# Optimization experiments

Measured on AMD Instinct MI355X. Metric: run time of the kernel, lower is better.

The kernel has to match this reference:

```python
import jax, jax.numpy as jnp
import numpy as np

H = 16
EPS = 1e-6
AUX_COEF = 0.01
TOPK = 2


def _rmsnorm(x, w):
    ms = jnp.mean(x * x, axis=-1, keepdims=True)
    return x * jax.lax.rsqrt(ms + EPS) * w


def _rope(t, cos, sin):
    # t: [B,H,T,hd]; cos/sin: [T, hd//2]
    half = t.shape[-1] // 2
    t1, t2 = t[..., :half], t[..., half:]
    return jnp.concatenate([t1 * cos - t2 * sin, t1 * sin + t2 * cos], axis=-1)


def setup_inputs() -> dict:
    key = jax.random.key(0)
    ks = jax.random.split(key, 16)
    B, T, D = 2, 1024, 1024
    E, I = 8, 4096
    s = lambda k, shp, fan: jax.random.normal(k, shp, dtype=jnp.float32) * (1.0 / np.sqrt(fan))
    return {
        "x": jax.random.normal(ks[0], (B, T, D), dtype=jnp.float32),
        "qkv_w": s(ks[1], (3 * D, D), D),
        "qkv_b": jnp.zeros((3 * D,), jnp.float32),
        "out_w": s(ks[2], (D, D), D),
        "out_b": jnp.zeros((D,), jnp.float32),
        "ln1_w": jnp.ones((D,), jnp.float32),
        "ln2_w": jnp.ones((D,), jnp.float32),
        "gate_w": s(ks[3], (E, D), D),
        "ew1": s(ks[4], (E, I, D), D),
        "eb1": jnp.zeros((E, I), jnp.float32),
        "ew2": s(ks[5], (E, D, I), I),
        "eb2": jnp.zeros((E, D), jnp.float32),
        "ew3": s(ks[6], (E, I, D), D),
        "eb3": jnp.zeros((E, I), jnp.float32),
    }


def _attention(x, qkv_w, qkv_b, out_w, out_b):
    B, T, D = x.shape
    hd = D // H
    half = hd // 2
    qkv = (x @ qkv_w.T + qkv_b).reshape(B, T, H, 3, hd)
    q = jnp.transpose(qkv[..., 0, :], (0, 2, 1, 3))  # [B,H,T,hd]
    k = jnp.transpose(qkv[..., 1, :], (0, 2, 1, 3))
    v = jnp.transpose(qkv[..., 2, :], (0, 2, 1, 3))
    theta = 1.0 / (10000.0 ** (jnp.arange(half, dtype=jnp.float32) / half))
    freq = jnp.arange(T, dtype=jnp.float32)[:, None] * theta[None, :]  # [T,half]
    cos, sin = jnp.cos(freq), jnp.sin(freq)
    q = _rope(q, cos, sin)
    k = _rope(k, cos, sin)
    # NOTE: original scales by embed_dim**-0.5 (not head_dim**-0.5)
    scale = D ** (-0.5)
    scores = jnp.einsum("bhqd,bhkd->bhqk", q, k) * scale
    mask = jnp.triu(jnp.full((T, T), -1e9, dtype=scores.dtype), k=1)
    w = jax.nn.softmax(scores + mask, axis=-1)
    attn = jnp.einsum("bhqk,bhkd->bhqd", w, v)
    attn = jnp.transpose(attn, (0, 2, 1, 3)).reshape(B, T, D)
    return attn @ out_w.T + out_b


def _moe(x, gate_w, ew1, eb1, ew2, eb2, ew3, eb3):
    B, T, D = x.shape
    E = gate_w.shape[0]
    xf = x.reshape(-1, D)  # [N,D]
    N = xf.shape[0]
    probs = jax.nn.softmax(xf @ gate_w.T, axis=-1)  # [N,E]
    topk_vals, topk_idx = jax.lax.top_k(probs, TOPK)
    oh = jax.nn.one_hot(topk_idx, E, dtype=xf.dtype)  # [N,K,E]
    gates = jnp.sum(oh * topk_vals[..., None], axis=1)  # [N,E] dense gate, zero off top-k
    # per-expert SwiGLU over all tokens, combined with sparse gates
    h = jax.nn.silu(jnp.einsum("nd,eid->nei", xf, ew1) + eb1) * (
        jnp.einsum("nd,eid->nei", xf, ew3) + eb3
    )  # [N,E,I]
    out_e = jnp.einsum("nei,edi->ned", h, ew2) + eb2  # [N,E,D]
    y = jnp.einsum("ned,ne->nd", out_e, gates)
    counts = jnp.sum(oh, axis=(0, 1))  # bincount of routed assignments
    f = counts / (N * TOPK)
    P = jnp.mean(probs, axis=0)
    aux = AUX_COEF * E * jnp.dot(f, P)
    return y.reshape(B, T, D), aux


def reference(x, qkv_w, qkv_b, out_w, out_b, ln1_w, ln2_w, gate_w, ew1, eb1, ew2, eb2, ew3, eb3):
    h1 = x + _attention(_rmsnorm(x, ln1_w), qkv_w, qkv_b, out_w, out_b)
    y, aux = _moe(_rmsnorm(h1, ln2_w), gate_w, ew1, eb1, ew2, eb2, ew3, eb3)
    return h1 + y, aux
```

## Files before the change

### kernel.cpp

```cpp
#include <hip/hip_runtime.h>
#include <cstdint>
#include <cstddef>
#include <math.h>

#define T_SEQ  1024
#define DMODEL 1024
#define NHEAD  16
#define HDIM   64
#define NEXP   8
#define IDIM   4096
#define NTOK   2048
#define NSLOT  4096

typedef short bf16x8 __attribute__((ext_vector_type(8)));
typedef short s16x4  __attribute__((ext_vector_type(4)));
typedef float floatx4 __attribute__((ext_vector_type(4)));
typedef unsigned int uintx4 __attribute__((ext_vector_type(4)));

__device__ __forceinline__ float bf2f(short s) {
  return __uint_as_float(((unsigned)(unsigned short)s) << 16);
}
__device__ __forceinline__ short f2bf(float f) {
  unsigned u = __float_as_uint(f);
  unsigned r = (u + 0x7FFFu + ((u >> 16) & 1u)) >> 16;
  return (short)r;
}
__device__ __forceinline__ unsigned cvt_pk_bf16(float lo, float hi) {
  unsigned r;
  asm("v_cvt_pk_bf16_f32 %0, %1, %2" : "=v"(r) : "v"(lo), "v"(hi));
  return r;
}
__device__ __forceinline__ uintx4 pack8_bf16(floatx4 a, floatx4 b) {
  uintx4 u;
  u[0] = cvt_pk_bf16(a[0], a[1]);
  u[1] = cvt_pk_bf16(a[2], a[3]);
  u[2] = cvt_pk_bf16(b[0], b[1]);
  u[3] = cvt_pk_bf16(b[2], b[3]);
  return u;
}
__device__ __forceinline__ void split8(const float* x, uintx4& hi, uintx4& lo) {
  #pragma unroll
  for (int i = 0; i < 4; i++) {
    unsigned h = cvt_pk_bf16(x[2*i], x[2*i+1]);
    hi[i] = h;
    float r0 = x[2*i]   - __uint_as_float(h << 16);
    float r1 = x[2*i+1] - __uint_as_float(h & 0xffff0000u);
    lo[i] = cvt_pk_bf16(r0, r1);
  }
}

__global__ __launch_bounds__(256) void rmsnorm_f32_kernel(
    const float* __restrict__ x, const float* __restrict__ w, float* __restrict__ out) {
  int row = blockIdx.x, tid = threadIdx.x;
  const floatx4* xr = (const floatx4*)(x + (size_t)row * DMODEL);
  floatx4 v = xr[tid];
  float ss = v[0]*v[0] + v[1]*v[1] + v[2]*v[2] + v[3]*v[3];
  #pragma unroll
  for (int off = 32; off > 0; off >>= 1) ss += __shfl_xor(ss, off);
  __shared__ float wsum[4];
  int wid = tid >> 6;
  if ((tid & 63) == 0) wsum[wid] = ss;
  __syncthreads();
  float tot = wsum[0] + wsum[1] + wsum[2] + wsum[3];
  float r = rsqrtf(tot * (1.0f / DMODEL) + 1e-6f);
  floatx4 wv = ((const floatx4*)w)[tid];
  floatx4 o;
  o[0] = v[0]*r*wv[0]; o[1] = v[1]*r*wv[1];
  o[2] = v[2]*r*wv[2]; o[3] = v[3]*r*wv[3];
  ((floatx4*)(out + (size_t)row * DMODEL))[tid] = o;
}

__global__ __launch_bounds__(256) void rmsnorm_bf16_kernel(
    const float* __restrict__ x, const float* __restrict__ w, short* __restrict__ out) {
  int row = blockIdx.x, tid = threadIdx.x;
  const floatx4* xr = (const floatx4*)(x + (size_t)row * DMODEL);
  floatx4 v = xr[tid];
  float ss = v[0]*v[0] + v[1]*v[1] + v[2]*v[2] + v[3]*v[3];
  #pragma unroll
  for (int off = 32; off > 0; off >>= 1) ss += __shfl_xor(ss, off);
  __shared__ float wsum[4];
  int wid = tid >> 6;
  if ((tid & 63) == 0) wsum[wid] = ss;
  __syncthreads();
  float tot = wsum[0] + wsum[1] + wsum[2] + wsum[3];
  float r = rsqrtf(tot * (1.0f / DMODEL) + 1e-6f);
  floatx4 wv = ((const floatx4*)w)[tid];
  s16x4 o;
  o[0] = f2bf(v[0]*r*wv[0]); o[1] = f2bf(v[1]*r*wv[1]);
  o[2] = f2bf(v[2]*r*wv[2]); o[3] = f2bf(v[3]*r*wv[3]);
  *(s16x4*)(out + (size_t)row * DMODEL + tid*4) = o;
}

template<int RESID>
__global__ __launch_bounds__(256) void gemm_3bf16(
    const float* __restrict__ A, const float* __restrict__ W,
    const float* __restrict__ bias, const float* __restrict__ resid,
    float* __restrict__ C, int N, int K) {
  __shared__ __attribute__((aligned(16))) short Ahi[2][64*40];
  __shared__ __attribute__((aligned(16))) short Alo[2][64*40];
  __shared__ __attribute__((aligned(16))) short Whi[2][64*40];
  __shared__ __attribute__((aligned(16))) short Wlo[2][64*40];
  int tid = threadIdx.x, lane = tid & 63, wid = tid >> 6;
  int wm = wid >> 1, wn = wid & 1;
  int m0 = blockIdx.y * 64, n0 = blockIdx.x * 64;
  floatx4 zero4 = {0.f,0.f,0.f,0.f};
  floatx4 acc[2][2];
  #pragma unroll
  for (int mi = 0; mi < 2; mi++)
    #pragma unroll
    for (int nj = 0; nj < 2; nj++) acc[mi][nj] = zero4;

  int ar = tid >> 2, ak = (tid & 3) * 8;
  const float* Ap = A + (size_t)(m0 + ar) * K + ak;
  const float* Wp = W + (size_t)(n0 + ar) * K + ak;
  int rsel = lane & 15, kseg = (lane >> 4) * 8;

  {
    float abuf[8], wbuf[8];
    *(floatx4*)(abuf)     = *(const floatx4*)(Ap);
    *(floatx4*)(abuf + 4) = *(const floatx4*)(Ap + 4);
    *(floatx4*)(wbuf)     = *(const floatx4*)(Wp);
    *(floatx4*)(wbuf + 4) = *(const floatx4*)(Wp + 4);
    uintx4 ahi, alo, whi, wlo;
    split8(abuf, ahi, alo);
    split8(wbuf, whi, wlo);
    *(uintx4*)(&Ahi[0][ar*40 + ak]) = ahi;
    *(uintx4*)(&Alo[0][ar*40 + ak]) = alo;
    *(uintx4*)(&Whi[0][ar*40 + ak]) = whi;
    *(uintx4*)(&Wlo[0][ar*40 + ak]) = wlo;
  }
  __syncthreads();

  for (int kk = 0; kk < K; kk += 32) {
    int cur = (kk >> 5) & 1;
    int nxt = cur ^ 1;
    bool more = (kk + 32 < K);
    float nab[8], nwb[8];
    if (more) {
      *(floatx4*)(nab)     = *(const floatx4*)(Ap + kk + 32);
      *(floatx4*)(nab + 4) = *(const floatx4*)(Ap + kk + 36);
      *(floatx4*)(nwb)     = *(const floatx4*)(Wp + kk + 32);
      *(floatx4*)(nwb + 4) = *(const floatx4*)(Wp + kk + 36);
    }
    bf16x8 afh[2], afl[2], wfh[2], wfl[2];
    #pragma unroll
    for (int mi = 0; mi < 2; mi++) {
      int row = (wm*32 + mi*16 + rsel)*40 + kseg;
      afh[mi] = *(const bf16x8*)(&Ahi[cur][row]);
      afl[mi] = *(const bf16x8*)(&Alo[cur][row]);
    }
    #pragma unroll
    for (int nj = 0; nj < 2; nj++) {
      int row = (wn*32 + nj*16 + rsel)*40 + kseg;
      wfh[nj] = *(const bf16x8*)(&Whi[cur][row]);
      wfl[nj] = *(const bf16x8*)(&Wlo[cur][row]);
    }
    #pragma unroll
    for (int mi = 0; mi < 2; mi++)
      #pragma unroll
      for (int nj = 0; nj < 2; nj++) {
        acc[mi][nj] = __builtin_amdgcn_mfma_f32_16x16x32_bf16(afl[mi], wfh[nj], acc[mi][nj], 0, 0, 0);
        acc[mi][nj] = __builtin_amdgcn_mfma_f32_16x16x32_bf16(afh[mi], wfl[nj], acc[mi][nj], 0, 0, 0);
        acc[mi][nj] = __builtin_amdgcn_mfma_f32_16x16x32_bf16(afh[mi], wfh[nj], acc[mi][nj], 0, 0, 0);
      }
    if (more) {
      uintx4 ahi, alo, whi, wlo;
      split8(nab, ahi, alo);
      split8(nwb, whi, wlo);
      *(uintx4*)(&Ahi[nxt][ar*40 + ak]) = ahi;
      *(uintx4*)(&Alo[nxt][ar*40 + ak]) = alo;
      *(uintx4*)(&Whi[nxt][ar*40 + ak]) = whi;
      *(uintx4*)(&Wlo[nxt][ar*40 + ak]) = wlo;
    }
    __syncthreads();
  }
  int rj = (lane >> 4) * 4, cn = lane & 15;
  #pragma unroll
  for (int mi = 0; mi < 2; mi++) {
    #pragma unroll
    for (int nj = 0; nj < 2; nj++) {
      int n = n0 + wn*32 + nj*16 + cn;
      float bn = bias[n];
      #pragma unroll
      for (int j = 0; j < 4; j++) {
        int m = m0 + wm*32 + mi*16 + rj + j;
        float v = acc[mi][nj][j] + bn;
        if (RESID) v += resid[(size_t)m * N + n];
        C[(size_t)m * N + n] = v;
      }
    }
  }
}

__global__ void rope_table_kernel(float* __restrict__ cost, float* __restrict__ sint) {
  int t = blockIdx.x, d = threadIdx.x;
  double theta = pow(10000.0, -(double)d / 32.0);
  double f = (double)t * theta;
  cost[t*32 + d] = (float)cos(f);
  sint[t*32 + d] = (float)sin(f);
}

__global__ __launch_bounds__(256) void rope_kernel(
    const float* __restrict__ qkv, const float* __restrict__ cost, const float* __restrict__ sint,
    float* __restrict__ qr, float* __restrict__ kr) {
  int wid = threadIdx.x >> 6, lane = threadIdx.x & 63;
  int idx = blockIdx.x * 4 + wid;
  int h = idx & 15, n = idx >> 4;
  int t = n & (T_SEQ - 1), b = n >> 10;
  const float* base = qkv + (size_t)n * 3072 + h * 192;
  int d2 = lane & 31;
  float c = cost[t*32 + d2], s = sint[t*32 + d2];
  float q1 = base[d2],      q2 = base[d2 + 32];
  float k1 = base[64 + d2], k2 = base[96 + d2];
  float qo = (lane < 32) ? (q1*c - q2*s) : (q1*s + q2*c);
  float ko = (lane < 32) ? (k1*c - k2*s) : (k1*s + k2*c);
  size_t orow = ((size_t)(b*NHEAD + h) * T_SEQ + t) * HDIM;
  qr[orow + lane] = qo;
  kr[orow + lane] = ko;
}

__global__ __launch_bounds__(256) void vtrans_kernel(
    const float* __restrict__ qkvf, float* __restrict__ vrT) {
  __shared__ __attribute__((aligned(16))) float tile[64][68];
  int bh = blockIdx.x, t0 = blockIdx.y * 64;
  int b = bh >> 4, h = bh & 15;
  int tid = threadIdx.x;
  int r = tid >> 2, seg = (tid & 3) * 16;
  const float* src = qkvf + ((size_t)(b*T_SEQ + t0 + r))*3072 + h*192 + 128 + seg;
  floatx4 v0 = *(const floatx4*)(src);
  floatx4 v1 = *(const floatx4*)(src + 4);
  floatx4 v2 = *(const floatx4*)(src + 8);
  floatx4 v3 = *(const floatx4*)(src + 12);
  *(floatx4*)(&tile[r][seg])      = v0;
  *(floatx4*)(&tile[r][seg + 4])  = v1;
  *(floatx4*)(&tile[r][seg + 8])  = v2;
  *(floatx4*)(&tile[r][seg + 12]) = v3;
  __syncthreads();
  int dr = r, tseg = seg;
  floatx4 o0, o1, o2, o3;
  #pragma unroll
  for (int i = 0; i < 4; i++) {
    o0[i] = tile[tseg + i][dr];
    o1[i] = tile[tseg + 4 + i][dr];
    o2[i] = tile[tseg + 8 + i][dr];
    o3[i] = tile[tseg + 12 + i][dr];
  }
  float* dst = vrT + ((size_t)(bh*HDIM + dr))*T_SEQ + t0 + tseg;
  *(floatx4*)(dst)      = o0;
  *(floatx4*)(dst + 4)  = o1;
  *(floatx4*)(dst + 8)  = o2;
  *(floatx4*)(dst + 12) = o3;
}

__global__ __launch_bounds__(256) void attn_mfma_kernel(
    const float* __restrict__ qr_, const float* __restrict__ kr_,
    const float* __restrict__ vrT_, float* __restrict__ attno) {
  __shared__ __attribute__((aligned(16))) short Qhi[64*72];
  __shared__ __attribute__((aligned(16))) short Qlo[64*72];
  __shared__ __attribute__((aligned(16))) short Khi[64*72];
  __shared__ __attribute__((aligned(16))) short Klo[64*72];
  __shared__ __attribute__((aligned(16))) short Vhi[64*72];
  __shared__ __attribute__((aligned(16))) short Vlo[64*72];
  __shared__ __attribute__((aligned(16))) unsigned Pp[64*68];
  int tid = threadIdx.x, lane = tid & 63, w = tid >> 6;
  int bh = blockIdx.x;
  int qt = 15 - (int)blockIdx.y;
  int q0 = qt * 64;
  int b = bh >> 4, h = bh & 15;
  const float* Qb  = qr_  + ((size_t)bh * T_SEQ + q0) * HDIM;
  const float* Kb  = kr_  + (size_t)bh * T_SEQ * HDIM;
  const float* Vtb = vrT_ + (size_t)bh * HDIM * T_SEQ;

  int srow = tid >> 2, sseg = (tid & 3) * 16;
  {
    const float* src = Qb + srow*HDIM + sseg;
    float b0[8], b1[8];
    *(floatx4*)(b0)   = *(const floatx4*)(src);
    *(floatx4*)(b0+4) = *(const floatx4*)(src + 4);
    *(floatx4*)(b1)   = *(const floatx4*)(src + 8);
    *(floatx4*)(b1+4) = *(const floatx4*)(src + 12);
    uintx4 h0, l0, h1, l1;
    split8(b0, h0, l0); split8(b1, h1, l1);
    *(uintx4*)(&Qhi[srow*72 + sseg])     = h0;
    *(uintx4*)(&Qhi[srow*72 + sseg + 8]) = h1;
    *(uintx4*)(&Qlo[srow*72 + sseg])     = l0;
    *(uintx4*)(&Qlo[srow*72 + sseg + 8]) = l1;
  }

  int rsel = lane & 15, kseg = (lane >> 4) * 8, cl = lane & 15;
  int rbase = w*16 + (lane >> 4) * 4;
  const float scale = 0.03125f;
  float mrow[4] = {-1e30f,-1e30f,-1e30f,-1e30f};
  float lrow[4] = {0.f,0.f,0.f,0.f};
  floatx4 zero4 = {0.f,0.f,0.f,0.f};
  floatx4 Of[4];
  #pragma unroll
  for (int f = 0; f < 4; f++) Of[f] = zero4;

  int ntiles = qt + 1;
  for (int kt = 0; kt < ntiles; kt++) {
    int kbase = kt << 6;
    const float* kp = Kb  + (size_t)(kbase + srow)*HDIM + sseg;
    const float* vp = Vtb + (size_t)srow*T_SEQ + kbase + sseg;
    float kb0[8], kb1[8], vb0[8], vb1[8];
    *(floatx4*)(kb0)   = *(const floatx4*)(kp);
    *(floatx4*)(kb0+4) = *(const floatx4*)(kp + 4);
    *(floatx4*)(kb1)   = *(const floatx4*)(kp + 8);
    *(floatx4*)(kb1+4) = *(const floatx4*)(kp + 12);
    *(floatx4*)(vb0)   = *(const floatx4*)(vp);
    *(floatx4*)(vb0+4) = *(const floatx4*)(vp + 4);
    *(floatx4*)(vb1)   = *(const floatx4*)(vp + 8);
    *(floatx4*)(vb1+4) = *(const floatx4*)(vp + 12);
    __syncthreads();
    {
      uintx4 h0, l0, h1, l1;
      split8(kb0, h0, l0); split8(kb1, h1, l1);
      *(uintx4*)(&Khi[srow*72 + sseg])     = h0;
      *(uintx4*)(&Khi[srow*72 + sseg + 8]) = h1;
      *(uintx4*)(&Klo[srow*72 + sseg])     = l0;
      *(uintx4*)(&Klo[srow*72 + sseg + 8]) = l1;
      split8(vb0, h0, l0); split8(vb1, h1, l1);
      *(uintx4*)(&Vhi[srow*72 + sseg])     = h0;
      *(uintx4*)(&Vhi[srow*72 + sseg + 8]) = h1;
      *(uintx4*)(&Vlo[srow*72 + sseg])     = l0;
      *(uintx4*)(&Vlo[srow*72 + sseg + 8]) = l1;
    }
    __syncthreads();
    floatx4 sf[4];
    #pragma unroll
    for (int f = 0; f < 4; f++) sf[f] = zero4;
    #pragma unroll
    for (int c = 0; c < 2; c++) {
      int ko = c*32 + kseg;
      bf16x8 qh = *(const bf16x8*)(&Qhi[(w*16 + rsel)*72 + ko]);
      bf16x8 ql = *(const bf16x8*)(&Qlo[(w*16 + rsel)*72 + ko]);
      #pragma unroll
      for (int f = 0; f < 4; f++) {
        bf16x8 kh = *(const bf16x8*)(&Khi[(f*16 + rsel)*72 + ko]);
        bf16x8 kl = *(const bf16x8*)(&Klo[(f*16 + rsel)*72 + ko]);
        sf[f] = __builtin_amdgcn_mfma_f32_16x16x32_bf16(ql, kh, sf[f], 0, 0, 0);
        sf[f] = __builtin_amdgcn_mfma_f32_16x16x32_bf16(qh, kl, sf[f], 0, 0, 0);
        sf[f] = __builtin_amdgcn_mfma_f32_16x16x32_bf16(qh, kh, sf[f], 0, 0, 0);
      }
    }
    float pm[4] = {-1e30f,-1e30f,-1e30f,-1e30f};
    #pragma unroll
    for (int f = 0; f < 4; f++) {
      int col = kbase + f*16 + cl;
      #pragma unroll
      for (int j = 0; j < 4; j++) {
        float s = sf[f][j];
        s = (col <= q0 + rbase + j) ? s*scale : -1e30f;
        sf[f][j] = s;
        pm[j] = fmaxf(pm[j], s);
      }
    }
    #pragma unroll
    for (int off = 1; off < 16; off <<= 1)
      #pragma unroll
      for (int j = 0; j < 4; j++) pm[j] = fmaxf(pm[j], __shfl_xor(pm[j], off));
    float sc[4], rs[4] = {0.f,0.f,0.f,0.f};
    #pragma unroll
    for (int j = 0; j < 4; j++) {
      float mn = fmaxf(mrow[j], pm[j]);
      sc[j] = __expf(mrow[j] - mn);
      mrow[j] = mn;
    }
    #pragma unroll
    for (int f = 0; f < 4; f++) {
      #pragma unroll
      for (int j = 0; j < 4; j++) {
        float p = (sf[f][j] > -1e29f) ? __expf(sf[f][j] - mrow[j]) : 0.f;
        rs[j] += p;
        unsigned hp = cvt_pk_bf16(p, 0.f);
        float ph = __uint_as_float(hp << 16);
        unsigned lp = cvt_pk_bf16(p - ph, 0.f);
        Pp[(rbase + j)*68 + f*16 + cl] = (hp << 16) | (lp & 0xffffu);
      }
    }
    #pragma unroll
    for (int off = 1; off < 16; off <<= 1)
      #pragma unroll
      for (int j = 0; j < 4; j++) rs[j] += __shfl_xor(rs[j], off);
    #pragma unroll
    for (int j = 0; j < 4; j++) lrow[j] = lrow[j]*sc[j] + rs[j];
    #pragma unroll
    for (int f = 0; f < 4; f++)
      #pragma unroll
      for (int j = 0; j < 4; j++) Of[f][j] *= sc[j];
    __syncthreads();
    #pragma unroll
    for (int c = 0; c < 2; c++) {
      int prow = (w*16 + rsel)*68 + c*32 + kseg;
      uintx4 d0 = *(const uintx4*)(&Pp[prow]);
      uintx4 d1 = *(const uintx4*)(&Pp[prow + 4]);
      uintx4 phw, plw;
      phw[0] = (d0[0] >> 16) | (d0[1] & 0xffff0000u);
      phw[1] = (d0[2] >> 16) | (d0[3] & 0xffff0000u);
      phw[2] = (d1[0] >> 16) | (d1[1] & 0xffff0000u);
      phw[3] = (d1[2] >> 16) | (d1[3] & 0xffff0000u);
      plw[0] = (d0[0] & 0xffffu) | (d0[1] << 16);
      plw[1] = (d0[2] & 0xffffu) | (d0[3] << 16);
      plw[2] = (d1[0] & 0xffffu) | (d1[1] << 16);
      plw[3] = (d1[2] & 0xffffu) | (d1[3] << 16);
      bf16x8 Ph = *(bf16x8*)&phw;
      bf16x8 Pl = *(bf16x8*)&plw;
      int ko = c*32 + kseg;
      #pragma unroll
      for (int f = 0; f < 4; f++) {
        bf16x8 vh = *(const bf16x8*)(&Vhi[(f*16 + rsel)*72 + ko]);
        bf16x8 vl = *(const bf16x8*)(&Vlo[(f*16 + rsel)*72 + ko]);
        Of[f] = __builtin_amdgcn_mfma_f32_16x16x32_bf16(Pl, vh, Of[f], 0, 0, 0);
        Of[f] = __builtin_amdgcn_mfma_f32_16x16x32_bf16(Ph, vl, Of[f], 0, 0, 0);
        Of[f] = __builtin_amdgcn_mfma_f32_16x16x32_bf16(Ph, vh, Of[f], 0, 0, 0);
      }
    }
  }
  #pragma unroll
  for (int j = 0; j < 4; j++) {
    float inv = 1.0f / lrow[j];
    size_t rowoff = ((size_t)(b*T_SEQ + q0 + rbase + j))*DMODEL + h*HDIM;
    #pragma unroll
    for (int f = 0; f < 4; f++)
      attno[rowoff + f*16 + cl] = Of[f][j] * inv;
  }
}

__global__ __launch_bounds__(64) void gate_kernel(
    const float* __restrict__ h1, const float* __restrict__ lnw, const float* __restrict__ gw,
    float* __restrict__ probs, int* __restrict__ pair, float* __restrict__ gpair,
    int* __restrict__ counts) {
  int n = blockIdx.x, lane = threadIdx.x;
  const float* xp = h1 + (size_t)n * DMODEL + lane*16;
  float xv[16];
  double ss = 0.0;
  #pragma unroll
  for (int j = 0; j < 16; j++) { xv[j] = xp[j]; ss += (double)xv[j] * (double)xv[j]; }
  #pragma unroll
  for (int off = 32; off > 0; off >>= 1) ss += __shfl_xor(ss, off);
  double r = 1.0 / sqrt(ss * (1.0 / DMODEL) + 1e-6);
  const float* wp = lnw + lane*16;
  double xf[16];
  #pragma unroll
  for (int j = 0; j < 16; j++) xf[j] = (double)xv[j] * r * (double)wp[j];
  double logit[8];
  #pragma unroll
  for (int e = 0; e < 8; e++) {
    const float* g = gw + e*DMODEL + lane*16;
    double acc = 0.0;
    #pragma unroll
    for (int j = 0; j < 16; j++) acc += xf[j] * (double)g[j];
    logit[e] = acc;
  }
  #pragma unroll
  for (int e = 0; e < 8; e++)
    #pragma unroll
    for (int off = 32; off > 0; off >>= 1) logit[e] += __shfl_xor(logit[e], off);
  double mxl = logit[0];
  #pragma unroll
  for (int e = 1; e < 8; e++) mxl = fmax(mxl, logit[e]);
  double p[8], Z = 0.0;
  #pragma unroll
  for (int e = 0; e < 8; e++) { p[e] = exp(logit[e] - mxl); Z += p[e]; }
  double invZ = 1.0 / Z;
  #pragma unroll
  for (int e = 0; e < 8; e++) p[e] *= invZ;
  int e0 = 0; double b0 = p[0];
  #pragma unroll
  for (int e = 1; e < 8; e++) if (p[e] > b0) { b0 = p[e]; e0 = e; }
  int e1 = -1; double b1 = -1.0;
  #pragma unroll
  for (int e = 0; e < 8; e++) if (e != e0 && p[e] > b1) { b1 = p[e]; e1 = e; }
  if (lane == 0) {
    #pragma unroll
    for (int e = 0; e < 8; e++) probs[n*8 + e] = (float)p[e];
    pair[2*n] = e0; pair[2*n+1] = e1;
    gpair[2*n] = (float)b0; gpair[2*n+1] = (float)b1;
    atomicAdd(&counts[e0], 1);
    atomicAdd(&counts[e1], 1);
  }
}

__global__ void offsets_kernel(const int* __restrict__ counts, int* __restrict__ off,
                               int* __restrict__ cursor) {
  if (threadIdx.x == 0) {
    int a = 0;
    for (int e = 0; e < 8; e++) { off[e] = a; cursor[e] = a; a += counts[e]; }
    off[8] = a;
  }
}

__global__ __launch_bounds__(256) void scatter_kernel(
    const int* __restrict__ pair, const float* __restrict__ gpair, int* __restrict__ cursor,
    int* __restrict__ tok_of_slot, float* __restrict__ gate_of_slot, int* __restrict__ slot_of_tok) {
  int n = blockIdx.x * 256 + threadIdx.x;
  int e0 = pair[2*n], e1 = pair[2*n+1];
  int s0 = atomicAdd(&cursor[e0], 1);
  tok_of_slot[s0] = n; gate_of_slot[s0] = gpair[2*n];   slot_of_tok[2*n] = s0;
  int s1 = atomicAdd(&cursor[e1], 1);
  tok_of_slot[s1] = n; gate_of_slot[s1] = gpair[2*n+1]; slot_of_tok[2*n+1] = s1;
}

__global__ __launch_bounds__(256) void aux_kernel(
    const float* __restrict__ probs, const int* __restrict__ counts, float* __restrict__ outaux) {
  __shared__ double sm[256];
  int t = threadIdx.x;
  int e = t & 7, base = t >> 3;
  double acc = 0.0;
  for (int n = base; n < NTOK; n += 32) acc += (double)probs[n*8 + e];
  sm[t] = acc;
  __syncthreads();
  if (t < 8) {
    double s = 0.0;
    for (int g = 0; g < 32; g++) s += sm[g*8 + t];
    sm[t] = s;
  }
  __syncthreads();
  if (t == 0) {
    double aux = 0.0;
    for (int ee = 0; ee < 8; ee++)
      aux += ((double)counts[ee] * (1.0 / (NTOK*2))) * (sm[ee] * (1.0 / NTOK));
    outaux[0] = (float)(0.08 * aux);
  }
}

__global__ __launch_bounds__(256) void moe13_kernel(
    const short* __restrict__ xn2,
    const float* __restrict__ ew1, const float* __restrict__ eb1,
    const float* __restrict__ ew3, const float* __restrict__ eb3,
    const int* __restrict__ counts, const int* __restrict__ off,
    const int* __restrict__ tok_of_slot, short* __restrict__ hbuf) {
  int e = blockIdx.z;
  int Me = counts[e];
  int m0 = blockIdx.y * 128;
  if (m0 >= Me) return;
  int base = off[e];
  int i0 = blockIdx.x * 64;
  __shared__ __attribute__((aligned(16))) short As[2][128*40];
  __shared__ __attribute__((aligned(16))) short W1s[2][64*40];
  __shared__ __attribute__((aligned(16))) short W3s[2][64*40];
  int tid = threadIdx.x, lane = tid & 63, wid = tid >> 6;
  int wm = wid >> 1, wn = wid & 1;
  floatx4 zero4 = {0.f,0.f,0.f,0.f};
  floatx4 acc1[4][2], acc3[4][2];
  #pragma unroll
  for (int mi = 0; mi < 4; mi++)
    #pragma unroll
    for (int nj = 0; nj < 2; nj++) { acc1[mi][nj] = zero4; acc3[mi][nj] = zero4; }

  int ar = tid >> 1, ak = (tid & 1) * 8;
  int am = m0 + ar;
  bool aval = (am < Me);
  const short* Ag = xn2 + (size_t)(aval ? tok_of_slot[base + am] : 0) * DMODEL;
  int wr = tid >> 2, wk = (tid & 3) * 8;
  const float* W1g = ew1 + ((size_t)e*IDIM + i0 + wr)*DMODEL + wk;
  const float* W3g = ew3 + ((size_t)e*IDIM + i0 + wr)*DMODEL + wk;
  int rsel = lane & 15, kseg = (lane >> 4) * 8;

  {
    bf16x8 a0 = {0,0,0,0,0,0,0,0}, a1 = {0,0,0,0,0,0,0,0};
    if (aval) {
      a0 = *(const bf16x8*)(Ag + ak);
      a1 = *(const bf16x8*)(Ag + ak + 16);
    }
    floatx4 u0 = *(const floatx4*)(W1g);
    floatx4 u1 = *(const floatx4*)(W1g + 4);
    floatx4 v0 = *(const floatx4*)(W3g);
    floatx4 v1 = *(const floatx4*)(W3g + 4);
    *(bf16x8*)(&As[0][ar*40 + ak])      = a0;
    *(bf16x8*)(&As[0][ar*40 + ak + 16]) = a1;
    *(uintx4*)(&W1s[0][wr*40 + wk]) = pack8_bf16(u0, u1);
    *(uintx4*)(&W3s[0][wr*40 + wk]) = pack8_bf16(v0, v1);
  }
  __syncthreads();

  for (int kk = 0; kk < DMODEL; kk += 32) {
    int cur = (kk >> 5) & 1;
    int nxt = cur ^ 1;
    bool more = (kk + 32 < DMODEL);
    bf16x8 na0 = {0,0,0,0,0,0,0,0}, na1 = {0,0,0,0,0,0,0,0};
    floatx4 nu0, nu1, nv0, nv1;
    if (more) {
      if (aval) {
        na0 = *(const bf16x8*)(Ag + kk + 32 + ak);
        na1 = *(const bf16x8*)(Ag + kk + 32 + ak + 16);
      }
      nu0 = *(const floatx4*)(W1g + kk + 32);
      nu1 = *(const floatx4*)(W1g + kk + 36);
      nv0 = *(const floatx4*)(W3g + kk + 32);
      nv1 = *(const floatx4*)(W3g + kk + 36);
    }
    bf16x8 af[4], w1f[2], w3f[2];
    #pragma unroll
    for (int mi = 0; mi < 4; mi++)
      af[mi] = *(const bf16x8*)(&As[cur][(wm*64 + mi*16 + rsel)*40 + kseg]);
    #pragma unroll
    for (int nj = 0; nj < 2; nj++) {
      w1f[nj] = *(const bf16x8*)(&W1s[cur][(wn*32 + nj*16 + rsel)*40 + kseg]);
      w3f[nj] = *(const bf16x8*)(&W3s[cur][(wn*32 + nj*16 + rsel)*40 + kseg]);
    }
    #pragma unroll
    for (int mi = 0; mi < 4; mi++)
      #pragma unroll
      for (int nj = 0; nj < 2; nj++) {
        acc1[mi][nj] = __builtin_amdgcn_mfma_f32_16x16x32_bf16(af[mi], w1f[nj], acc1[mi][nj], 0, 0, 0);
        acc3[mi][nj] = __builtin_amdgcn_mfma_f32_16x16x32_bf16(af[mi], w3f[nj], acc3[mi][nj], 0, 0, 0);
      }
    if (more) {
      *(bf16x8*)(&As[nxt][ar*40 + ak])      = na0;
      *(bf16x8*)(&As[nxt][ar*40 + ak + 16]) = na1;
      *(uintx4*)(&W1s[nxt][wr*40 + wk]) = pack8_bf16(nu0, nu1);
      *(uintx4*)(&W3s[nxt][wr*40 + wk]) = pack8_bf16(nv0, nv1);
    }
    __syncthreads();
  }
  int rj = (lane >> 4) * 4, cn = lane & 15;
  #pragma unroll
  for (int mi = 0; mi < 4; mi++) {
    #pragma unroll
    for (int nj = 0; nj < 2; nj++) {
      int i = i0 + wn*32 + nj*16 + cn;
      float be1 = eb1[e*IDIM + i], be3 = eb3[e*IDIM + i];
      #pragma unroll
      for (int j = 0; j < 4; j++) {
        int m = m0 + wm*64 + mi*16 + rj + j;
        if (m < Me) {
          float a = acc1[mi][nj][j] + be1;
          float b = acc3[mi][nj][j] + be3;
          float hval = (a / (1.f + __expf(-a))) * b;
          hbuf[(size_t)(base + m)*IDIM + i] = f2bf(hval);
        }
      }
    }
  }
}

__global__ __launch_bounds__(256) void moe2_kernel(
    const short* __restrict__ hbuf, const float* __restrict__ ew2, const float* __restrict__ eb2,
    const int* __restrict__ counts, const int* __restrict__ off,
    const float* __restrict__ gate_of_slot,
    float* __restrict__ y0, float* __restrict__ y1) {
  int e = blockIdx.z;
  int Me = counts[e];
  int m0 = blockIdx.y * 128;
  if (m0 >= Me) return;
  int base = off[e];
  int n0 = (blockIdx.x & 7) * 128;
  int khalf = blockIdx.x >> 3;
  int kbeg = khalf * (IDIM/2);
  __shared__ __attribute__((aligned(16))) short As[2][128*40];
  __shared__ __attribute__((aligned(16))) short Ws[2][128*40];
  int tid = threadIdx.x, lane = tid & 63, wid = tid >> 6;
  int wm = wid >> 1, wn = wid & 1;
  floatx4 zero4 = {0.f,0.f,0.f,0.f};
  floatx4 acc[4][4];
  #pragma unroll
  for (int mi = 0; mi < 4; mi++)
    #pragma unroll
    for (int nj = 0; nj < 4; nj++) acc[mi][nj] = zero4;

  int ar = tid >> 1, ak = (tid & 1) * 8, kw = (tid & 1) * 16;
  bool aval = (m0 + ar) < Me;
  const short* Ag = hbuf + (size_t)(base + (aval ? (m0 + ar) : 0)) * IDIM + kbeg;
  const float* Wg = ew2 + ((size_t)e*DMODEL + n0 + ar)*IDIM + kbeg;
  int rsel = lane & 15, kseg = (lane >> 4) * 8;

  {
    bf16x8 a0 = {0,0,0,0,0,0,0,0}, a1 = {0,0,0,0,0,0,0,0};
    if (aval) {
      a0 = *(const bf16x8*)(Ag + ak);
      a1 = *(const bf16x8*)(Ag + ak + 16);
    }
    floatx4 w0 = *(const floatx4*)(Wg + kw);
    floatx4 w1 = *(const floatx4*)(Wg + kw + 4);
    floatx4 w2 = *(const floatx4*)(Wg + kw + 8);
    floatx4 w3 = *(const floatx4*)(Wg + kw + 12);
    *(bf16x8*)(&As[0][ar*40 + ak])      = a0;
    *(bf16x8*)(&As[0][ar*40 + ak + 16]) = a1;
    *(uintx4*)(&Ws[0][ar*40 + kw])     = pack8_bf16(w0, w1);
    *(uintx4*)(&Ws[0][ar*40 + kw + 8]) = pack8_bf16(w2, w3);
  }
  __syncthreads();

  for (int kk = 0; kk < IDIM/2; kk += 32) {
    int cur = (kk >> 5) & 1;
    int nxt = cur ^ 1;
    bool more = (kk + 32 < IDIM/2);
    bf16x8 na0 = {0,0,0,0,0,0,0,0}, na1 = {0,0,0,0,0,0,0,0};
    floatx4 nw0, nw1, nw2, nw3;
    if (more) {
      if (aval) {
        na0 = *(const bf16x8*)(Ag + kk + 32 + ak);
        na1 = *(const bf16x8*)(Ag + kk + 32 + ak + 16);
      }
      nw0 = *(const floatx4*)(Wg + kk + 32 + kw);
      nw1 = *(const floatx4*)(Wg + kk + 32 + kw + 4);
      nw2 = *(const floatx4*)(Wg + kk + 32 + kw + 8);
      nw3 = *(const floatx4*)(Wg + kk + 32 + kw + 12);
    }
    bf16x8 af[4], wf[4];
    #pragma unroll
    for (int mi = 0; mi < 4; mi++)
      af[mi] = *(const bf16x8*)(&As[cur][(wm*64 + mi*16 + rsel)*40 + kseg]);
    #pragma unroll
    for (int nj = 0; nj < 4; nj++)
      wf[nj] = *(const bf16x8*)(&Ws[cur][(wn*64 + nj*16 + rsel)*40 + kseg]);
    #pragma unroll
    for (int mi = 0; mi < 4; mi++)
      #pragma unroll
      for (int nj = 0; nj < 4; nj++)
        acc[mi][nj] = __builtin_amdgcn_mfma_f32_16x16x32_bf16(af[mi], wf[nj], acc[mi][nj], 0, 0, 0);
    if (more) {
      *(bf16x8*)(&As[nxt][ar*40 + ak])      = na0;
      *(bf16x8*)(&As[nxt][ar*40 + ak + 16]) = na1;
      *(uintx4*)(&Ws[nxt][ar*40 + kw])     = pack8_bf16(nw0, nw1);
      *(uintx4*)(&Ws[nxt][ar*40 + kw + 8]) = pack8_bf16(nw2, nw3);
    }
    __syncthreads();
  }
  int rj = (lane >> 4) * 4, cn = lane & 15;
  float* yout = khalf ? y1 : y0;
  #pragma unroll
  for (int mi = 0; mi < 4; mi++) {
    #pragma unroll
    for (int nj = 0; nj < 4; nj++) {
      int n = n0 + wn*64 + nj*16 + cn;
      float bn = khalf ? 0.f : eb2[e*DMODEL + n];
      #pragma unroll
      for (int j = 0; j < 4; j++) {
        int m = m0 + wm*64 + mi*16 + rj + j;
        if (m < Me) {
          float g = gate_of_slot[base + m];
          yout[(size_t)(base + m)*DMODEL + n] = (acc[mi][nj][j] + bn) * g;
        }
      }
    }
  }
}

__global__ __launch_bounds__(256) void combine_kernel(
    const float* __restrict__ h1, const float* __restrict__ y0, const float* __restrict__ y1,
    const int* __restrict__ slot_of_tok, float* __restrict__ out) {
  int n = blockIdx.x, t = threadIdx.x;
  int sA = slot_of_tok[2*n], sB = slot_of_tok[2*n+1];
  const floatx4* a   = (const floatx4*)(h1 + (size_t)n*DMODEL);
  const floatx4* y0a = (const floatx4*)(y0 + (size_t)sA*DMODEL);
  const floatx4* y1a = (const floatx4*)(y1 + (size_t)sA*DMODEL);
  const floatx4* y0b = (const floatx4*)(y0 + (size_t)sB*DMODEL);
  const floatx4* y1b = (const floatx4*)(y1 + (size_t)sB*DMODEL);
  floatx4 v = a[t] + (y0a[t] + y1a[t]) + (y0b[t] + y1b[t]);
  ((floatx4*)(out + (size_t)n*DMODEL))[t] = v;
}

extern "C" void kernel_launch(void* const* d_in, const int* in_sizes, int n_in,
                              void* d_out, int out_size, void* d_ws, size_t ws_size,
                              hipStream_t stream) {
  const float* x      = (const float*)d_in[0];
  const float* qkv_w  = (const float*)d_in[1];
  const float* qkv_b  = (const float*)d_in[2];
  const float* out_w  = (const float*)d_in[3];
  const float* out_b  = (const float*)d_in[4];
  const float* ln1_w  = (const float*)d_in[5];
  const float* ln2_w  = (const float*)d_in[6];
  const float* gate_w = (const float*)d_in[7];
  const float* ew1    = (const float*)d_in[8];
  const float* eb1    = (const float*)d_in[9];
  const float* ew2    = (const float*)d_in[10];
  const float* eb2    = (const float*)d_in[11];
  const float* ew3    = (const float*)d_in[12];
  const float* eb3    = (const float*)d_in[13];
  float* out = (float*)d_out;

  char* ws = (char*)d_ws;
  float* xn1f   = (float*)(ws + 0);
  float* attnof = (float*)(ws + 0);
  float* qkvf   = (float*)(ws + 8388608);
  float* h1     = (float*)(ws + 8388608);
  short* xn2    = (short*)(ws + 16777216);
  float* yslot1 = (float*)(ws + 16777216);
  float* qrf    = (float*)(ws + 33554432);
  float* krf    = (float*)(ws + 41943040);
  float* vrT    = (float*)(ws + 50331648);
  short* hbuf   = (short*)(ws + 33554432);
  float* yslot0 = (float*)(ws + 67108864);
  float* cost         = (float*)(ws + 83886080);
  float* sint         = (float*)(ws + 84017152);
  float* probs        = (float*)(ws + 84148224);
  int*   ctrl         = (int*)  (ws + 84213760);
  int*   pair         = (int*)  (ws + 84214784);
  float* gpair        = (float*)(ws + 84231168);
  int*   slot_of_tok  = (int*)  (ws + 84247552);
  int*   tok_of_slot  = (int*)  (ws + 84263936);
  float* gate_of_slot = (float*)(ws + 84280320);

  int* counts = ctrl;
  int* off    = ctrl + 8;
  int* cursor = ctrl + 20;

  hipMemsetAsync(ctrl, 0, 1024, stream);
  rope_table_kernel<<<T_SEQ, 32, 0, stream>>>(cost, sint);
  rmsnorm_f32_kernel<<<NTOK, 256, 0, stream>>>(x, ln1_w, xn1f);
  gemm_3bf16<0><<<dim3(48, 32), 256, 0, stream>>>(xn1f, qkv_w, qkv_b, nullptr, qkvf, 3072, DMODEL);
  rope_kernel<<<8192, 256, 0, stream>>>(qkvf, cost, sint, qrf, krf);
  vtrans_kernel<<<dim3(32, 16), 256, 0, stream>>>(qkvf, vrT);
  attn_mfma_kernel<<<dim3(32, 16), 256, 0, stream>>>(qrf, krf, vrT, attnof);
  gemm_3bf16<1><<<dim3(16, 32), 256, 0, stream>>>(attnof, out_w, out_b, x, h1, DMODEL, DMODEL);
  rmsnorm_bf16_kernel<<<NTOK, 256, 0, stream>>>(h1, ln2_w, xn2);
  gate_kernel<<<NTOK, 64, 0, stream>>>(h1, ln2_w, gate_w, probs, pair, gpair, counts);
  offsets_kernel<<<1, 64, 0, stream>>>(counts, off, cursor);
  scatter_kernel<<<8, 256, 0, stream>>>(pair, gpair, cursor, tok_of_slot, gate_of_slot, slot_of_tok);
  aux_kernel<<<1, 256, 0, stream>>>(probs, counts, out + 2097152);
  moe13_kernel<<<dim3(64, 16, 8), 256, 0, stream>>>(xn2, ew1, eb1, ew3, eb3, counts, off, tok_of_slot, hbuf);
  moe2_kernel<<<dim3(16, 16, 8), 256, 0, stream>>>(hbuf, ew2, eb2, counts, off, gate_of_slot, yslot0, yslot1);
  combine_kernel<<<NTOK, 256, 0, stream>>>(h1, yslot0, yslot1, slot_of_tok, out);
}
```

Baseline: 536.1 us.

## Pre-split fp32 operands into bf16 hi/lo planes before attention GEMMs

Adds a split kernel that converts the QKV and output projection weights into bf16 hi/lo arrays once per call. RMSNorm and the attention epilogue now emit hi/lo bf16 directly, and the GEMM loads pre-split bf16 tiles instead of converting fp32 inside the K loop. This removes the repeated split arithmetic that each GEMM block did on the same tiles, at the cost of extra launches and extra workspace traffic for the split weights.

After: 541.4 us. About the same (+1.0%).

```diff
diff --git a/kernel.cpp b/kernel.cpp
--- a/kernel.cpp
+++ b/kernel.cpp
@@ -49,25 +49,46 @@
   }
 }
 
-__global__ __launch_bounds__(256) void rmsnorm_f32_kernel(
-    const float* __restrict__ x, const float* __restrict__ w, float* __restrict__ out) {
+__global__ __launch_bounds__(256) void split_kernel(
+    const float* __restrict__ src, short* __restrict__ hi, short* __restrict__ lo, int n8) {
+  int i = blockIdx.x * 256 + threadIdx.x;
+  if (i >= n8) return;
+  float buf[8];
+  *(floatx4*)(buf)     = *(const floatx4*)(src + (size_t)i*8);
+  *(floatx4*)(buf + 4) = *(const floatx4*)(src + (size_t)i*8 + 4);
+  uintx4 h, l;
+  split8(buf, h, l);
+  *(uintx4*)(hi + (size_t)i*8) = h;
+  *(uintx4*)(lo + (size_t)i*8) = l;
+}
+
+__global__ __launch_bounds__(128) void rmsnorm_split_kernel(
+    const float* __restrict__ x, const float* __restrict__ w,
+    short* __restrict__ hi, short* __restrict__ lo) {
   int row = blockIdx.x, tid = threadIdx.x;
-  const floatx4* xr = (const floatx4*)(x + (size_t)row * DMODEL);
-  floatx4 v = xr[tid];
-  float ss = v[0]*v[0] + v[1]*v[1] + v[2]*v[2] + v[3]*v[3];
+  const float* xr = x + (size_t)row * DMODEL + tid*8;
+  float v[8];
+  *(floatx4*)(v)     = *(const floatx4*)(xr);
+  *(floatx4*)(v + 4) = *(const floatx4*)(xr + 4);
+  float ss = 0.f;
+  #pragma unroll
+  for (int j = 0; j < 8; j++) ss += v[j]*v[j];
   #pragma unroll
   for (int off = 32; off > 0; off >>= 1) ss += __shfl_xor(ss, off);
-  __shared__ float wsum[4];
-  int wid = tid >> 6;
-  if ((tid & 63) == 0) wsum[wid] = ss;
+  __shared__ float ws2[2];
+  int wv = tid >> 6;
+  if ((tid & 63) == 0) ws2[wv] = ss;
   __syncthreads();
-  float tot = wsum[0] + wsum[1] + wsum[2] + wsum[3];
+  float tot = ws2[0] + ws2[1];
   float r = rsqrtf(tot * (1.0f / DMODEL) + 1e-6f);
-  floatx4 wv = ((const floatx4*)w)[tid];
-  floatx4 o;
-  o[0] = v[0]*r*wv[0]; o[1] = v[1]*r*wv[1];
-  o[2] = v[2]*r*wv[2]; o[3] = v[3]*r*wv[3];
-  ((floatx4*)(out + (size_t)row * DMODEL))[tid] = o;
+  const float* wp = w + tid*8;
+  float o[8];
+  #pragma unroll
+  for (int j = 0; j < 8; j++) o[j] = v[j]*r*wp[j];
+  uintx4 h, l;
+  split8(o, h, l);
+  *(uintx4*)(hi + (size_t)row * DMODEL + tid*8) = h;
+  *(uintx4*)(lo + (size_t)row * DMODEL + tid*8) = l;
 }
 
 __global__ __launch_bounds__(256) void rmsnorm_bf16_kernel(
@@ -92,8 +113,9 @@
 }
 
 template<int RESID>
-__global__ __launch_bounds__(256) void gemm_3bf16(
-    const float* __restrict__ A, const float* __restrict__ W,
+__global__ __launch_bounds__(256) void gemm_pre3(
+    const short* __restrict__ Ahi_g, const short* __restrict__ Alo_g,
+    const short* __restrict__ Whi_g, const short* __restrict__ Wlo_g,
     const float* __restrict__ bias, const float* __restrict__ resid,
     float* __restrict__ C, int N, int K) {
   __shared__ __attribute__((aligned(16))) short Ahi[2][64*40];
@@ -111,23 +133,21 @@
     for (int nj = 0; nj < 2; nj++) acc[mi][nj] = zero4;
 
   int ar = tid >> 2, ak = (tid & 3) * 8;
-  const float* Ap = A + (size_t)(m0 + ar) * K + ak;
-  const float* Wp = W + (size_t)(n0 + ar) * K + ak;
+  const short* Aph = Ahi_g + (size_t)(m0 + ar) * K + ak;
+  const short* Apl = Alo_g + (size_t)(m0 + ar) * K + ak;
+  const short* Wph = Whi_g + (size_t)(n0 + ar) * K + ak;
+  const short* Wpl = Wlo_g + (size_t)(n0 + ar) * K + ak;
   int rsel = lane & 15, kseg = (lane >> 4) * 8;
 
   {
-    float abuf[8], wbuf[8];
-    *(floatx4*)(abuf)     = *(const floatx4*)(Ap);
-    *(floatx4*)(abuf + 4) = *(const floatx4*)(Ap + 4);
-    *(floatx4*)(wbuf)     = *(const floatx4*)(Wp);
-    *(floatx4*)(wbuf + 4) = *(const floatx4*)(Wp + 4);
-    uintx4 ahi, alo, whi, wlo;
-    split8(abuf, ahi, alo);
-    split8(wbuf, whi, wlo);
-    *(uintx4*)(&Ahi[0][ar*40 + ak]) = ahi;
-    *(uintx4*)(&Alo[0][ar*40 + ak]) = alo;
-    *(uintx4*)(&Whi[0][ar*40 + ak]) = whi;
-    *(uintx4*)(&Wlo[0][ar*40 + ak]) = wlo;
+    bf16x8 ah = *(const bf16x8*)(Aph);
+    bf16x8 al = *(const bf16x8*)(Apl);
+    bf16x8 wh = *(const bf16x8*)(Wph);
+    bf16x8 wl = *(const bf16x8*)(Wpl);
+    *(bf16x8*)(&Ahi[0][ar*40 + ak]) = ah;
+    *(bf16x8*)(&Alo[0][ar*40 + ak]) = al;
+    *(bf16x8*)(&Whi[0][ar*40 + ak]) = wh;
+    *(bf16x8*)(&Wlo[0][ar*40 + ak]) = wl;
   }
   __syncthreads();
 
@@ -135,12 +155,13 @@
     int cur = (kk >> 5) & 1;
     int nxt = cur ^ 1;
     bool more = (kk + 32 < K);
-    float nab[8], nwb[8];
+    bf16x8 nah = {0,0,0,0,0,0,0,0}, nal = {0,0,0,0,0,0,0,0};
+    bf16x8 nwh = {0,0,0,0,0,0,0,0}, nwl = {0,0,0,0,0,0,0,0};
     if (more) {
-      *(floatx4*)(nab)     = *(const floatx4*)(Ap + kk + 32);
-      *(floatx4*)(nab + 4) = *(const floatx4*)(Ap + kk + 36);
-      *(floatx4*)(nwb)     = *(const floatx4*)(Wp + kk + 32);
-      *(floatx4*)(nwb + 4) = *(const floatx4*)(Wp + kk + 36);
+      nah = *(const bf16x8*)(Aph + kk + 32);
+      nal = *(const bf16x8*)(Apl + kk + 32);
+      nwh = *(const bf16x8*)(Wph + kk + 32);
+      nwl = *(const bf16x8*)(Wpl + kk + 32);
     }
     bf16x8 afh[2], afl[2], wfh[2], wfl[2];
     #pragma unroll
@@ -164,13 +185,10 @@
         acc[mi][nj] = __builtin_amdgcn_mfma_f32_16x16x32_bf16(afh[mi], wfh[nj], acc[mi][nj], 0, 0, 0);
       }
     if (more) {
-      uintx4 ahi, alo, whi, wlo;
-      split8(nab, ahi, alo);
-      split8(nwb, whi, wlo);
-      *(uintx4*)(&Ahi[nxt][ar*40 + ak]) = ahi;
-      *(uintx4*)(&Alo[nxt][ar*40 + ak]) = alo;
-      *(uintx4*)(&Whi[nxt][ar*40 + ak]) = whi;
-      *(uintx4*)(&Wlo[nxt][ar*40 + ak]) = wlo;
+      *(bf16x8*)(&Ahi[nxt][ar*40 + ak]) = nah;
+      *(bf16x8*)(&Alo[nxt][ar*40 + ak]) = nal;
+      *(bf16x8*)(&Whi[nxt][ar*40 + ak]) = nwh;
+      *(bf16x8*)(&Wlo[nxt][ar*40 + ak]) = nwl;
     }
     __syncthreads();
   }
@@ -254,7 +272,7 @@
 
 __global__ __launch_bounds__(256) void attn_mfma_kernel(
     const float* __restrict__ qr_, const float* __restrict__ kr_,
-    const float* __restrict__ vrT_, float* __restrict__ attno) {
+    const float* __restrict__ vrT_, short* __restrict__ attnhi, short* __restrict__ attnlo) {
   __shared__ __attribute__((aligned(16))) short Qhi[64*72];
   __shared__ __attribute__((aligned(16))) short Qlo[64*72];
   __shared__ __attribute__((aligned(16))) short Khi[64*72];
@@ -421,8 +439,14 @@
     float inv = 1.0f / lrow[j];
     size_t rowoff = ((size_t)(b*T_SEQ + q0 + rbase + j))*DMODEL + h*HDIM;
     #pragma unroll
-    for (int f = 0; f < 4; f++)
-      attno[rowoff + f*16 + cl] = Of[f][j] * inv;
+    for (int f = 0; f < 4; f++) {
+      float val = Of[f][j] * inv;
+      unsigned hp = cvt_pk_bf16(val, 0.f);
+      float ph = __uint_as_float(hp << 16);
+      unsigned lp = cvt_pk_bf16(val - ph, 0.f);
+      attnhi[rowoff + f*16 + cl] = (short)hp;
+      attnlo[rowoff + f*16 + cl] = (short)lp;
+    }
   }
 }
 
@@ -772,12 +796,18 @@
   float* out = (float*)d_out;
 
   char* ws = (char*)d_ws;
-  float* xn1f   = (float*)(ws + 0);
-  float* attnof = (float*)(ws + 0);
   float* qkvf   = (float*)(ws + 8388608);
   float* h1     = (float*)(ws + 8388608);
   short* xn2    = (short*)(ws + 16777216);
   float* yslot1 = (float*)(ws + 16777216);
+  short* attnhi = (short*)(ws + 16777216);
+  short* attnlo = (short*)(ws + 20971520);
+  short* outwhi = (short*)(ws + 25165824);
+  short* outwlo = (short*)(ws + 27262976);
+  short* xn1hi  = (short*)(ws + 33554432);
+  short* xn1lo  = (short*)(ws + 37748736);
+  short* qkvwhi = (short*)(ws + 41943040);
+  short* qkvwlo = (short*)(ws + 48234496);
   float* qrf    = (float*)(ws + 33554432);
   float* krf    = (float*)(ws + 41943040);
   float* vrT    = (float*)(ws + 50331648);
@@ -799,12 +829,14 @@
 
   hipMemsetAsync(ctrl, 0, 1024, stream);
   rope_table_kernel<<<T_SEQ, 32, 0, stream>>>(cost, sint);
-  rmsnorm_f32_kernel<<<NTOK, 256, 0, stream>>>(x, ln1_w, xn1f);
-  gemm_3bf16<0><<<dim3(48, 32), 256, 0, stream>>>(xn1f, qkv_w, qkv_b, nullptr, qkvf, 3072, DMODEL);
+  rmsnorm_split_kernel<<<NTOK, 128, 0, stream>>>(x, ln1_w, xn1hi, xn1lo);
+  split_kernel<<<1536, 256, 0, stream>>>(qkv_w, qkvwhi, qkvwlo, 3072*1024/8);
+  gemm_pre3<0><<<dim3(48, 32), 256, 0, stream>>>(xn1hi, xn1lo, qkvwhi, qkvwlo, qkv_b, nullptr, qkvf, 3072, DMODEL);
   rope_kernel<<<8192, 256, 0, stream>>>(qkvf, cost, sint, qrf, krf);
   vtrans_kernel<<<dim3(32, 16), 256, 0, stream>>>(qkvf, vrT);
-  attn_mfma_kernel<<<dim3(32, 16), 256, 0, stream>>>(qrf, krf, vrT, attnof);
-  gemm_3bf16<1><<<dim3(16, 32), 256, 0, stream>>>(attnof, out_w, out_b, x, h1, DMODEL, DMODEL);
+  attn_mfma_kernel<<<dim3(32, 16), 256, 0, stream>>>(qrf, krf, vrT, attnhi, attnlo);
+  split_kernel<<<512, 256, 0, stream>>>(out_w, outwhi, outwlo, 1024*1024/8);
+  gemm_pre3<1><<<dim3(16, 32), 256, 0, stream>>>(attnhi, attnlo, outwhi, outwlo, out_b, x, h1, DMODEL, DMODEL);
   rmsnorm_bf16_kernel<<<NTOK, 256, 0, stream>>>(h1, ln2_w, xn2);
   gate_kernel<<<NTOK, 64, 0, stream>>>(h1, ln2_w, gate_w, probs, pair, gpair, counts);
   offsets_kernel<<<1, 64, 0, stream>>>(counts, off, cursor);
```
